# Optimization experiments

Hardware: AMD Instinct MI355X
Metric: run time of the kernel (lower is better)

Reference implementation:

```python
import jax
import jax.numpy as jnp
from jax import lax
import numpy as np

B, T, IN, H, K = 8, 4096, 512, 512, 2


def setup_inputs() -> dict:
    key = jax.random.key(0)
    k = jax.random.split(key, 5)
    scale_w0 = 1.0 / np.sqrt(IN * K)
    scale_w1 = 1.0 / np.sqrt(H * K)
    return {
        "x": jax.random.normal(k[0], (B, T, IN), jnp.float32),
        "w0": jax.random.normal(k[1], (3 * H, IN, K), jnp.float32) * scale_w0,
        "b0": jax.random.normal(k[2], (3 * H,), jnp.float32) * scale_w0,
        "w1": jax.random.normal(k[3], (3 * H, H, K), jnp.float32) * scale_w1,
        "b1": jax.random.normal(k[4], (3 * H,), jnp.float32) * scale_w1,
    }


def _qrnn_layer(x, w, b):
    # x: [B, T, C]; w: [3H, C, K]; causal conv (left pad K-1), matching
    # torch padding=K-1 then slicing off the last K-1 timesteps.
    xc = jnp.transpose(x, (0, 2, 1))  # [B, C, T]
    conv = lax.conv_general_dilated(
        xc, w, window_strides=(1,), padding=[(K - 1, 0)],
        dimension_numbers=("NCH", "OIH", "NCH"))
    conv = conv + b[None, :, None]
    conv = jnp.transpose(conv, (0, 2, 1))  # [B, T, 3H]
    z, f, o = jnp.split(conv, 3, axis=-1)
    z = jnp.tanh(z)
    f = jax.nn.sigmoid(f)
    o = jax.nn.sigmoid(o)

    def step(h, zfo):
        zt, ft, ot = zfo
        h = ft * h + (1.0 - ft) * zt  # fo-pool recurrence
        return h, ot * h

    h0 = jnp.zeros((x.shape[0], z.shape[-1]), x.dtype)
    hT, outs = lax.scan(
        step, h0,
        (jnp.swapaxes(z, 0, 1), jnp.swapaxes(f, 0, 1), jnp.swapaxes(o, 0, 1)))
    return jnp.swapaxes(outs, 0, 1), hT  # [B, T, H], [B, H]


def reference(x, w0, b0, w1, b1):
    out, h0 = _qrnn_layer(x, w0, b0)
    out, h1 = _qrnn_layer(out, w1, b1)
    return out, h0, h1
```

## Files before the change

kernel.cpp:

```cpp
#include <hip/hip_runtime.h>
#include <cstdint>

#define B_ 8
#define T_ 4096
#define TP1 4097
#define IN_ 512
#define H_ 512
#define N3H 1536
#define KD 1024
#define CHUNKS 64
#define CLEN 64
#define NT 16

typedef __attribute__((ext_vector_type(4))) float floatx4;
typedef __attribute__((ext_vector_type(4))) float f4;
typedef __attribute__((ext_vector_type(8))) short short8;
typedef __attribute__((ext_vector_type(4))) unsigned short us4;
typedef __attribute__((ext_vector_type(4))) _Float16 h4;

__device__ __forceinline__ unsigned short f2bf(float v){
  unsigned int u = __float_as_uint(v);
  unsigned int r = (u + 0x7fffu + ((u >> 16) & 1u)) >> 16;
  return (unsigned short)r;
}
__device__ __forceinline__ float sigm(float x){
  return __builtin_amdgcn_rcpf(1.f + __expf(-x));
}
__device__ __forceinline__ float tanhf_(float x){ return 2.f*sigm(2.f*x) - 1.f; }

#define GLLS(src, dst) __builtin_amdgcn_global_load_lds( \
    (const __attribute__((address_space(1))) void*)(src), \
    (__attribute__((address_space(3))) void*)(dst), 16, 0, 0)

__global__ void cast_pad_kernel(const float* __restrict__ x, unsigned short* __restrict__ xpad){
  int64_t i = (int64_t)blockIdx.x*256 + threadIdx.x;
  const int64_t total = (int64_t)B_*TP1*(IN_/4);
  if (i >= total) return;
  int cg = (int)(i & 127);
  int64_t r = i >> 7;
  int t = (int)(r % TP1);
  int b = (int)(r / TP1);
  us4 o;
  if (t == 0){ o = (us4){0,0,0,0}; }
  else {
    f4 v = *(const f4*)(x + ((int64_t)b*T_ + (t-1))*IN_ + cg*4);
    #pragma unroll
    for (int u=0;u<4;++u) o[u] = f2bf(v[u]);
  }
  *(us4*)(xpad + r*IN_ + cg*4) = o;
}

__global__ void wt_kernel(const float* __restrict__ wA, unsigned short* __restrict__ wtA,
                          const float* __restrict__ wB, unsigned short* __restrict__ wtB){
  int i = blockIdx.x*256 + threadIdx.x;
  if (i >= N3H*512) return;
  const float* w = blockIdx.y ? wB : wA;
  unsigned short* wt = blockIdx.y ? wtB : wtA;
  int ci = i & 511;
  int o = i >> 9;
  const float* wp = w + (int64_t)o*KD + ci*2;
  wt[(int64_t)o*KD + ci]       = f2bf(wp[0]);
  wt[(int64_t)o*KD + 512 + ci] = f2bf(wp[1]);
}

#define MFMA(a,b,c) __builtin_amdgcn_mfma_f32_16x16x32_bf16(a,b,c,0,0,0)
#define BAR() __builtin_amdgcn_s_barrier()

#define ST_A(tt, h) do { \
    const unsigned short* _s = aSrc + (h)*128*IN_ + (tt)*64; \
    unsigned short* _d = smem + ((tt)&1)*16384 + (h)*8192 + dstBase; \
    GLLS(_s, _d); GLLS(_s + 64*IN_, _d + 4096); } while(0)
#define ST_B(tt, h) do { \
    const unsigned short* _s = bSrc + (h)*128*KD + (tt)*64; \
    unsigned short* _d = smem + 32768 + ((tt)&1)*16384 + (h)*8192 + dstBase; \
    GLLS(_s, _d); GLLS(_s + 64*KD, _d + 4096); } while(0)

#define LDA(d,h,i,s) (*(const short8*)(smem + (d)*16384 + (h)*8192 + aRd + (i)*1024 + (s)))
#define LDB(d,h,i,s) (*(const short8*)(smem + (d)*16384 + (h)*8192 + bRd + (i)*1024 + (s)))

#define TILE(tc, SA1, SB1, SA0, SB0, VMN) do { \
  const int d_ = (tc) & 1; \
   \
  _Pragma("unroll") for (int i=0;i<4;++i){ aF[i][0]=LDA(d_,0,i,sw0); aF[i][1]=LDA(d_,0,i,sw1); } \
  _Pragma("unroll") for (int j=0;j<2;++j){ bF0[j][0]=LDB(d_,0,j,sw0); bF0[j][1]=LDB(d_,0,j,sw1); } \
  if (SA1) ST_A((tc)+1, 1); \
  BAR(); \
  __builtin_amdgcn_s_setprio(1); \
  _Pragma("unroll") for (int i=0;i<4;++i) _Pragma("unroll") for (int j=0;j<2;++j){ \
    acc[i][j]=MFMA(aF[i][0],bF0[j][0],acc[i][j]); acc[i][j]=MFMA(aF[i][1],bF0[j][1],acc[i][j]); } \
  __builtin_amdgcn_s_setprio(0); \
  BAR(); \
   \
  _Pragma("unroll") for (int j=0;j<2;++j){ bF1[j][0]=LDB(d_,1,j,sw0); bF1[j][1]=LDB(d_,1,j,sw1); } \
  if (SB1) ST_B((tc)+1, 1); \
  BAR(); \
  __builtin_amdgcn_s_setprio(1); \
  _Pragma("unroll") for (int i=0;i<4;++i) _Pragma("unroll") for (int j=0;j<2;++j){ \
    acc[i][2+j]=MFMA(aF[i][0],bF1[j][0],acc[i][2+j]); acc[i][2+j]=MFMA(aF[i][1],bF1[j][1],acc[i][2+j]); } \
  __builtin_amdgcn_s_setprio(0); \
  BAR(); \
   \
  _Pragma("unroll") for (int i=0;i<4;++i){ aF[i][0]=LDA(d_,1,i,sw0); aF[i][1]=LDA(d_,1,i,sw1); } \
  if (SA0) ST_A((tc)+2, 0); \
  BAR(); \
  __builtin_amdgcn_s_setprio(1); \
  _Pragma("unroll") for (int i=0;i<4;++i) _Pragma("unroll") for (int j=0;j<2;++j){ \
    acc[4+i][j]=MFMA(aF[i][0],bF0[j][0],acc[4+i][j]); acc[4+i][j]=MFMA(aF[i][1],bF0[j][1],acc[4+i][j]); } \
  __builtin_amdgcn_s_setprio(0); \
  BAR(); \
   \
  if (SB0) ST_B((tc)+2, 0); \
  BAR(); \
  __builtin_amdgcn_s_setprio(1); \
  _Pragma("unroll") for (int i=0;i<4;++i) _Pragma("unroll") for (int j=0;j<2;++j){ \
    acc[4+i][2+j]=MFMA(aF[i][0],bF1[j][0],acc[4+i][2+j]); acc[4+i][2+j]=MFMA(aF[i][1],bF1[j][1],acc[4+i][2+j]); } \
  __builtin_amdgcn_s_setprio(0); \
  if ((VMN)==4) asm volatile("s_waitcnt vmcnt(4)" ::: "memory"); \
  else if ((VMN)==0) asm volatile("s_waitcnt vmcnt(0)" ::: "memory"); \
  BAR(); \
} while(0)

__global__ __launch_bounds__(512, 2) void gemm_kernel(
    const unsigned short* __restrict__ A, const unsigned short* __restrict__ W,
    const float* __restrict__ bias, _Float16* __restrict__ C){
  __shared__ unsigned short smem[65536];
  const int tid  = threadIdx.x;
  const int lane = tid & 63;
  const int wave = tid >> 6;
  const int l16  = lane & 15;
  const int quad = lane >> 4;
  const int wm = wave >> 2;
  const int wn = wave & 3;
  const int lrow = lane >> 3;
  const int lcol = lane & 7;

  const int bid = blockIdx.x;
  const int wg = (bid & 7) * 96 + (bid >> 3);
  const int mt = wg / 6;
  const int nt = wg % 6;
  const int m0 = mt * 256;
  const int n0 = nt * 256;
  const int bb = m0 / T_;
  const int act = n0 >> 9;

  const unsigned short* aSrc = A + (int64_t)(m0 + bb + wave*8 + lrow)*IN_ + (lcol ^ lrow)*8;
  const unsigned short* bSrc = W + (int64_t)(n0 + wave*8 + lrow)*KD + (lcol ^ lrow)*8;
  const int dstBase = (wave*8 + lrow)*64 + lcol*8;

  const int sw0 = ( quad      ^ (l16 & 7)) * 8;
  const int sw1 = ((4 ^ quad) ^ (l16 & 7)) * 8;
  const int aRd = (wm*64 + l16)*64;
  const int bRd = 32768 + (wn*32 + l16)*64;

  floatx4 acc[8][4];
  #pragma unroll
  for (int i=0;i<8;i++)
    #pragma unroll
    for (int j=0;j<4;j++) acc[i][j] = (floatx4){0.f,0.f,0.f,0.f};
  short8 aF[4][2], bF0[2][2], bF1[2][2];

  ST_A(0,0); ST_B(0,0); ST_A(0,1); ST_B(0,1); ST_A(1,0); ST_B(1,0);
  asm volatile("s_waitcnt vmcnt(4)" ::: "memory");
  BAR();

  #pragma unroll 2
  for (int t = 0; t < NT-2; ++t){
    TILE(t, 1, 1, 1, 1, 4);
  }
  TILE(NT-2, 1, 1, 0, 0, 0);
  TILE(NT-1, 0, 0, 0, 0, -1);

  float bv[4];
  #pragma unroll
  for (int n=0;n<4;++n){
    const int cb = ((n&2)?128:0) + wn*32 + (n&1)*16;
    bv[n] = bias[n0 + cb + l16];
  }
  #pragma unroll
  for (int m=0;m<8;++m){
    const int rb = ((m&4)?128:0) + wm*64 + (m&3)*16;
    const int row = m0 + rb + quad*4;
    #pragma unroll
    for (int n=0;n<4;++n){
      const int cb = ((n&2)?128:0) + wn*32 + (n&1)*16;
      const int col = n0 + cb + l16;
      _Float16* cp = C + (int64_t)row*N3H + col;
      #pragma unroll
      for (int r=0;r<4;++r){
        float v = acc[m][n][r] + bv[n];
        v = (act == 0) ? tanhf_(v) : sigm(v);
        cp[(int64_t)r*N3H] = (_Float16)v;
      }
    }
  }
}

__global__ void scan_phase1(const _Float16* __restrict__ conv,
                            float* __restrict__ carA, float* __restrict__ carB){
  int q = blockIdx.x*256 + threadIdx.x;
  int chg = q & 127;
  int bq = (q >> 7) & 7;
  int c  = q >> 10;
  int ch = chg*4;
  f4 Aa = {1.f,1.f,1.f,1.f}, Bb = {0.f,0.f,0.f,0.f};
  const _Float16* p = conv + ((int64_t)bq*T_ + c*CLEN)*N3H + ch;
  for (int g=0; g<CLEN/8; ++g){
    h4 zb[8], fb[8];
    #pragma unroll
    for (int u=0;u<8;++u){
      zb[u] = *(const h4*)(p + (int64_t)u*N3H);
      fb[u] = *(const h4*)(p + (int64_t)u*N3H + 512);
    }
    #pragma unroll
    for (int u=0;u<8;++u){
      #pragma unroll
      for (int v=0;v<4;++v){
        float fv = (float)fb[u][v];
        float zv = (float)zb[u][v];
        Aa[v] *= fv;
        Bb[v] = fv*Bb[v] + (1.f-fv)*zv;
      }
    }
    p += (int64_t)8*N3H;
  }
  *(f4*)(carA + (int64_t)q*4) = Aa;
  *(f4*)(carB + (int64_t)q*4) = Bb;
}

__global__ void scan_phase2(const float* __restrict__ carA, const float* __restrict__ carB,
                            float* __restrict__ hstart, float* __restrict__ hT){
  int q = blockIdx.x*64 + threadIdx.x;
  float h = 0.f;
  for (int c0=0;c0<CHUNKS;c0+=8){
    float a[8], b[8];
    #pragma unroll
    for (int u=0;u<8;++u){
      a[u] = carA[(int64_t)(c0+u)*4096 + q];
      b[u] = carB[(int64_t)(c0+u)*4096 + q];
    }
    #pragma unroll
    for (int u=0;u<8;++u){
      hstart[(int64_t)(c0+u)*4096 + q] = h;
      h = a[u]*h + b[u];
    }
  }
  hT[q] = h;
}

template<int LAYER>
__global__ void scan_phase3(const _Float16* __restrict__ conv,
                            const float* __restrict__ hstart, unsigned short* __restrict__ xpad,
                            float* __restrict__ outf){
  int q = blockIdx.x*256 + threadIdx.x;
  int chg = q & 127;
  int bq = (q >> 7) & 7;
  int c  = q >> 10;
  int ch = chg*4;
  f4 h;
  #pragma unroll
  for (int v=0;v<4;++v) h[v] = hstart[(int64_t)c*4096 + bq*512 + ch + v];
  const _Float16* p = conv + ((int64_t)bq*T_ + c*CLEN)*N3H + ch;
  int t = c*CLEN;
  for (int g=0; g<CLEN/8; ++g){
    h4 zb[8], fb[8], ob[8];
    #pragma unroll
    for (int u=0;u<8;++u){
      zb[u] = *(const h4*)(p + (int64_t)u*N3H);
      fb[u] = *(const h4*)(p + (int64_t)u*N3H + 512);
      ob[u] = *(const h4*)(p + (int64_t)u*N3H + 1024);
    }
    #pragma unroll
    for (int u=0;u<8;++u){
      if (LAYER == 0){
        us4 ov4;
        #pragma unroll
        for (int v=0;v<4;++v){
          float fv = (float)fb[u][v];
          h[v] = fv*h[v] + (1.f-fv)*(float)zb[u][v];
          ov4[v] = f2bf((float)ob[u][v]*h[v]);
        }
        *(us4*)(xpad + ((int64_t)bq*TP1 + t+u + 1)*IN_ + ch) = ov4;
      } else {
        f4 of4;
        #pragma unroll
        for (int v=0;v<4;++v){
          float fv = (float)fb[u][v];
          h[v] = fv*h[v] + (1.f-fv)*(float)zb[u][v];
          of4[v] = (float)ob[u][v]*h[v];
        }
        *(f4*)(outf + ((int64_t)bq*T_ + t+u)*H_ + ch) = of4;
      }
    }
    t += 8; p += (int64_t)8*N3H;
  }
}

extern "C" void kernel_launch(void* const* d_in, const int* in_sizes, int n_in,
                              void* d_out, int out_size, void* d_ws, size_t ws_size,
                              hipStream_t stream){
  const float* x  = (const float*)d_in[0];
  const float* w0 = (const float*)d_in[1];
  const float* b0 = (const float*)d_in[2];
  const float* w1 = (const float*)d_in[3];
  const float* b1 = (const float*)d_in[4];
  float* out = (float*)d_out;

  char* ws = (char*)d_ws;
  size_t off = 0;
  auto alloc = [&](size_t bytes)->char*{
    char* p = ws + off; off = (off + bytes + 255) & ~(size_t)255; return p; };
  unsigned short* xpad = (unsigned short*)alloc((size_t)B_*TP1*IN_*2);
  unsigned short* Wt0  = (unsigned short*)alloc((size_t)N3H*KD*2);
  unsigned short* Wt1  = (unsigned short*)alloc((size_t)N3H*KD*2);
  _Float16* conv = (_Float16*)alloc((size_t)B_*T_*N3H*2);
  float* carA = (float*)alloc((size_t)CHUNKS*4096*4);
  float* carB = (float*)alloc((size_t)CHUNKS*4096*4);
  float* hst  = (float*)alloc((size_t)CHUNKS*4096*4);
  if (off > ws_size) return;

  float* out_main = out;
  float* h0 = out + (int64_t)B_*T_*H_;
  float* h1 = h0 + B_*H_;

  const int64_t padN = (int64_t)B_*TP1*(IN_/4);
  cast_pad_kernel<<<(int)((padN + 255)/256), 256, 0, stream>>>(x, xpad);
  dim3 wgrid((N3H*512 + 255)/256, 2);
  wt_kernel<<<wgrid, 256, 0, stream>>>(w0, Wt0, w1, Wt1);

  const int ggrid = ((B_*T_)/256) * (N3H/256);
  const int sgrid = (CHUNKS*8*128) / 256;
  gemm_kernel<<<ggrid, 512, 0, stream>>>(xpad, Wt0, b0, conv);
  scan_phase1<<<sgrid, 256, 0, stream>>>(conv, carA, carB);
  scan_phase2<<<64, 64, 0, stream>>>(carA, carB, hst, h0);
  scan_phase3<0><<<sgrid, 256, 0, stream>>>(conv, hst, xpad, nullptr);

  gemm_kernel<<<ggrid, 512, 0, stream>>>(xpad, Wt1, b1, conv);
  scan_phase1<<<sgrid, 256, 0, stream>>>(conv, carA, carB);
  scan_phase2<<<64, 64, 0, stream>>>(carA, carB, hst, h1);
  scan_phase3<1><<<sgrid, 256, 0, stream>>>(conv, hst, nullptr, out_main);
}
```

Baseline: 435.1 us.

## Fold chunk-carry scan into phase 3 and merge prep kernels

Removes the serial scan_phase2 kernel. Each phase-3 thread now recomputes its chunk's starting hidden state by folding the carries of all preceding chunks, and the last chunk writes hT. It also merges the input cast/pad and weight cast kernels into one prep launch. This drops two launches per layer and the hstart buffer, but it adds redundant carry reads and FMAs that grow with the chunk index. That adds load imbalance across blocks.

```diff
diff --git a/kernel.cpp b/kernel.cpp
--- a/kernel.cpp
+++ b/kernel.cpp
@@ -32,35 +32,36 @@
     (const __attribute__((address_space(1))) void*)(src), \
     (__attribute__((address_space(3))) void*)(dst), 16, 0, 0)
 
-__global__ void cast_pad_kernel(const float* __restrict__ x, unsigned short* __restrict__ xpad){
+__global__ void prep_kernel(const float* __restrict__ x, unsigned short* __restrict__ xpad,
+                            const float* __restrict__ w0, unsigned short* __restrict__ Wt0,
+                            const float* __restrict__ w1, unsigned short* __restrict__ Wt1){
   int64_t i = (int64_t)blockIdx.x*256 + threadIdx.x;
-  const int64_t total = (int64_t)B_*TP1*(IN_/4);
-  if (i >= total) return;
-  int cg = (int)(i & 127);
-  int64_t r = i >> 7;
-  int t = (int)(r % TP1);
-  int b = (int)(r / TP1);
-  us4 o;
-  if (t == 0){ o = (us4){0,0,0,0}; }
-  else {
-    f4 v = *(const f4*)(x + ((int64_t)b*T_ + (t-1))*IN_ + cg*4);
-    #pragma unroll
-    for (int u=0;u<4;++u) o[u] = f2bf(v[u]);
-  }
-  *(us4*)(xpad + r*IN_ + cg*4) = o;
-}
-
-__global__ void wt_kernel(const float* __restrict__ wA, unsigned short* __restrict__ wtA,
-                          const float* __restrict__ wB, unsigned short* __restrict__ wtB){
-  int i = blockIdx.x*256 + threadIdx.x;
-  if (i >= N3H*512) return;
-  const float* w = blockIdx.y ? wB : wA;
-  unsigned short* wt = blockIdx.y ? wtB : wtA;
-  int ci = i & 511;
-  int o = i >> 9;
-  const float* wp = w + (int64_t)o*KD + ci*2;
-  wt[(int64_t)o*KD + ci]       = f2bf(wp[0]);
-  wt[(int64_t)o*KD + 512 + ci] = f2bf(wp[1]);
+  const int64_t castN = (int64_t)B_*TP1*(IN_/4);
+  if (i < castN){
+    int cg = (int)(i & 127);
+    int64_t r = i >> 7;
+    int t = (int)(r % TP1);
+    int b = (int)(r / TP1);
+    us4 o;
+    if (t == 0){ o = (us4){0,0,0,0}; }
+    else {
+      f4 v = *(const f4*)(x + ((int64_t)b*T_ + (t-1))*IN_ + cg*4);
+      #pragma unroll
+      for (int u=0;u<4;++u) o[u] = f2bf(v[u]);
+    }
+    *(us4*)(xpad + r*IN_ + cg*4) = o;
+  } else {
+    int64_t j = i - castN;
+    int layer = (j >= (int64_t)N3H*512);
+    int jj = (int)(j - (int64_t)layer*N3H*512);
+    const float* w = layer ? w1 : w0;
+    unsigned short* wt = layer ? Wt1 : Wt0;
+    int ci = jj & 511;
+    int o = jj >> 9;
+    const float* wp = w + (int64_t)o*KD + ci*2;
+    wt[(int64_t)o*KD + ci]       = f2bf(wp[0]);
+    wt[(int64_t)o*KD + 512 + ci] = f2bf(wp[1]);
+  }
 }
 
 #define MFMA(a,b,c) __builtin_amdgcn_mfma_f32_16x16x32_bf16(a,b,c,0,0,0)
@@ -227,38 +228,47 @@
   *(f4*)(carB + (int64_t)q*4) = Bb;
 }
 
-__global__ void scan_phase2(const float* __restrict__ carA, const float* __restrict__ carB,
-                            float* __restrict__ hstart, float* __restrict__ hT){
-  int q = blockIdx.x*64 + threadIdx.x;
-  float h = 0.f;
-  for (int c0=0;c0<CHUNKS;c0+=8){
-    float a[8], b[8];
-    #pragma unroll
-    for (int u=0;u<8;++u){
-      a[u] = carA[(int64_t)(c0+u)*4096 + q];
-      b[u] = carB[(int64_t)(c0+u)*4096 + q];
-    }
-    #pragma unroll
-    for (int u=0;u<8;++u){
-      hstart[(int64_t)(c0+u)*4096 + q] = h;
-      h = a[u]*h + b[u];
-    }
-  }
-  hT[q] = h;
-}
-
 template<int LAYER>
 __global__ void scan_phase3(const _Float16* __restrict__ conv,
-                            const float* __restrict__ hstart, unsigned short* __restrict__ xpad,
-                            float* __restrict__ outf){
+                            const float* __restrict__ carA, const float* __restrict__ carB,
+                            float* __restrict__ hT,
+                            unsigned short* __restrict__ xpad, float* __restrict__ outf){
   int q = blockIdx.x*256 + threadIdx.x;
   int chg = q & 127;
   int bq = (q >> 7) & 7;
   int c  = q >> 10;
   int ch = chg*4;
-  f4 h;
-  #pragma unroll
-  for (int v=0;v<4;++v) h[v] = hstart[(int64_t)c*4096 + bq*512 + ch + v];
+  const int base = bq*128 + chg;
+
+  f4 h = {0.f,0.f,0.f,0.f};
+  {
+    int j = 0;
+    for (; j+8 <= c; j += 8){
+      f4 a[8], b[8];
+      #pragma unroll
+      for (int u=0;u<8;++u){
+        a[u] = *(const f4*)(carA + (int64_t)((j+u)*1024 + base)*4);
+        b[u] = *(const f4*)(carB + (int64_t)((j+u)*1024 + base)*4);
+      }
+      #pragma unroll
+      for (int u=0;u<8;++u)
+        #pragma unroll
+        for (int v=0;v<4;++v) h[v] = a[u][v]*h[v] + b[u][v];
+    }
+    for (; j < c; ++j){
+      f4 a = *(const f4*)(carA + (int64_t)(j*1024 + base)*4);
+      f4 b = *(const f4*)(carB + (int64_t)(j*1024 + base)*4);
+      #pragma unroll
+      for (int v=0;v<4;++v) h[v] = a[v]*h[v] + b[v];
+    }
+  }
+  if (c == CHUNKS-1){
+    f4 a = *(const f4*)(carA + (int64_t)((CHUNKS-1)*1024 + base)*4);
+    f4 b = *(const f4*)(carB + (int64_t)((CHUNKS-1)*1024 + base)*4);
+    #pragma unroll
+    for (int v=0;v<4;++v) hT[bq*512 + ch + v] = a[v]*h[v] + b[v];
+  }
+
   const _Float16* p = conv + ((int64_t)bq*T_ + c*CLEN)*N3H + ch;
   int t = c*CLEN;
   for (int g=0; g<CLEN/8; ++g){
@@ -315,27 +325,23 @@
   _Float16* conv = (_Float16*)alloc((size_t)B_*T_*N3H*2);
   float* carA = (float*)alloc((size_t)CHUNKS*4096*4);
   float* carB = (float*)alloc((size_t)CHUNKS*4096*4);
-  float* hst  = (float*)alloc((size_t)CHUNKS*4096*4);
   if (off > ws_size) return;
 
   float* out_main = out;
   float* h0 = out + (int64_t)B_*T_*H_;
   float* h1 = h0 + B_*H_;
 
-  const int64_t padN = (int64_t)B_*TP1*(IN_/4);
-  cast_pad_kernel<<<(int)((padN + 255)/256), 256, 0, stream>>>(x, xpad);
-  dim3 wgrid((N3H*512 + 255)/256, 2);
-  wt_kernel<<<wgrid, 256, 0, stream>>>(w0, Wt0, w1, Wt1);
+  const int64_t castN = (int64_t)B_*TP1*(IN_/4);
+  const int64_t prepN = castN + (int64_t)2*N3H*512;
+  prep_kernel<<<(int)((prepN + 255)/256), 256, 0, stream>>>(x, xpad, w0, Wt0, w1, Wt1);
 
   const int ggrid = ((B_*T_)/256) * (N3H/256);
   const int sgrid = (CHUNKS*8*128) / 256;
   gemm_kernel<<<ggrid, 512, 0, stream>>>(xpad, Wt0, b0, conv);
   scan_phase1<<<sgrid, 256, 0, stream>>>(conv, carA, carB);
-  scan_phase2<<<64, 64, 0, stream>>>(carA, carB, hst, h0);
-  scan_phase3<0><<<sgrid, 256, 0, stream>>>(conv, hst, xpad, nullptr);
+  scan_phase3<0><<<sgrid, 256, 0, stream>>>(conv, carA, carB, h0, xpad, nullptr);
 
   gemm_kernel<<<ggrid, 512, 0, stream>>>(xpad, Wt1, b1, conv);
   scan_phase1<<<sgrid, 256, 0, stream>>>(conv, carA, carB);
-  scan_phase2<<<64, 64, 0, stream>>>(carA, carB, hst, h1);
-  scan_phase3<1><<<sgrid, 256, 0, stream>>>(conv, hst, nullptr, out_main);
-}
+  scan_phase3<1><<<sgrid, 256, 0, stream>>>(conv, carA, carB, h1, nullptr, out_main);
+}
```

Result: faster. 405.6 us (median of 2 runs) (-6.8%).
